# Optimization experiments

Measured on AMD Instinct MI355X. Metric: run time of the kernel, lower is better.

## Reference

```python
import jax, jax.numpy as jnp
import numpy as np

N, C_IN, C_OUT, W_DIM, H, W = 16, 512, 512, 512, 64, 64

def setup_inputs() -> dict:
    key = jax.random.key(0)
    ks = jax.random.split(key, 6)
    return {
        "x": jax.random.normal(ks[0], (N, C_IN, H, W), dtype=jnp.float32),
        "w": jax.random.normal(ks[1], (N, W_DIM), dtype=jnp.float32),
        "noise": jax.random.normal(ks[2], (N, 1, H, W), dtype=jnp.float32),
        "affine_w": jax.random.normal(ks[3], (C_IN, W_DIM), dtype=jnp.float32) * (1.0 / np.sqrt(W_DIM)),
        "affine_b": jnp.ones((C_IN,), dtype=jnp.float32),  # bias_init=1.0
        "noise_strength": jnp.ones((), dtype=jnp.float32),
        "conv_w": jax.random.normal(ks[4], (C_OUT, C_IN, 3, 3), dtype=jnp.float32),
        "conv_b": jnp.zeros((C_OUT,), dtype=jnp.float32),
    }

def reference(x, w, noise, affine_w, affine_b, noise_strength, conv_w, conv_b):
    # affine: s = w @ affine_w.T + affine_b  (no activation)
    s = jnp.einsum('nd,cd->nc', w, affine_w) + affine_b  # [N, C_in]
    # Demodulated per-sample conv. Original builds w_n = W * s_n then demodulates;
    # since conv is linear in the weight's input-channel scale, this is equivalent to
    # scaling the input by s and the output by the demod factor d.
    w2 = jnp.sum(conv_w * conv_w, axis=(2, 3))  # [O, I]: sum over kernel taps
    d = jax.lax.rsqrt(jnp.einsum('ni,oi->no', s * s, w2) + 1e-8)  # [N, O]
    x_mod = x * s[:, :, None, None]
    y = jax.lax.conv_general_dilated(
        x_mod, conv_w, window_strides=(1, 1), padding='SAME',
        dimension_numbers=('NCHW', 'OIHW', 'NCHW'))  # [N, O, H, W]
    y = y * d[:, :, None, None] + conv_b[None, :, None, None]
    y = y + noise * noise_strength
    return jnp.where(y >= 0, y, 0.2 * y)  # LeakyReLU(0.2)
```

## Files before the change

kernel.cpp:

```cpp
#include <hip/hip_runtime.h>
#include <hip/hip_bf16.h>

typedef unsigned short u16;
typedef short bf16x8 __attribute__((ext_vector_type(8)));
typedef float f32x4 __attribute__((ext_vector_type(4)));

#define N_    16
#define CIN   512
#define COUT  512
#define WD    512
#define P_    4096
#define CC    (COUT * CIN)

#define OFF_S   0u
#define OFF_D   32768u
#define OFF_Z   65536u
#define OFF_WBT 131072u
#define OFF_XB  8388608u
#define WS_NEED (OFF_XB + 67108864u)

__device__ __forceinline__ u16 f2bf(float f) {
  union { float f; unsigned u; } a; a.f = f;
  unsigned r = a.u + 0x7fffu + ((a.u >> 16) & 1u);
  return (u16)(r >> 16);
}

__device__ __forceinline__ void gl_lds16(const u16* g, u16* l) {
  __builtin_amdgcn_global_load_lds(
      (const __attribute__((address_space(1))) void*)g,
      (__attribute__((address_space(3))) void*)l, 16, 0, 0);
}

__global__ void k_zero(float* z) { z[threadIdx.x] = 0.f; }

__global__ __launch_bounds__(256) void k_affine(const float* __restrict__ w,
                                                const float* __restrict__ aw,
                                                const float* __restrict__ ab,
                                                float* __restrict__ s) {
  int idx = blockIdx.x * 256 + threadIdx.x;
  int n = idx >> 9, c = idx & 511;
  const float4* wr = (const float4*)(w + (size_t)n * WD);
  const float4* ar = (const float4*)(aw + (size_t)c * WD);
  float acc = 0.f;
#pragma unroll 4
  for (int k = 0; k < WD / 4; ++k) {
    float4 a = wr[k], b = ar[k];
    acc += a.x * b.x + a.y * b.y + a.z * b.z + a.w * b.w;
  }
  s[idx] = acc + ab[c];
}

__global__ __launch_bounds__(256) void k_demod(const float* __restrict__ s,
                                               const float* __restrict__ cw,
                                               float* __restrict__ d) {
  __shared__ float w2[CIN];
  int o = blockIdx.x;
  const float* wr = cw + (size_t)o * CIN * 9;
  for (int i = threadIdx.x; i < CIN; i += 256) {
    float acc = 0.f;
#pragma unroll
    for (int t = 0; t < 9; ++t) { float v = wr[i * 9 + t]; acc += v * v; }
    w2[i] = acc;
  }
  __syncthreads();
  int wave = threadIdx.x >> 6, lane = threadIdx.x & 63;
  for (int nn = wave; nn < N_; nn += 4) {
    float acc = 0.f;
    for (int i = lane; i < CIN; i += 64) {
      float sv = s[nn * CIN + i];
      acc += sv * sv * w2[i];
    }
#pragma unroll
    for (int off = 32; off > 0; off >>= 1) acc += __shfl_down(acc, off);
    if (lane == 0) {
      float a = acc + 1e-8f;
      float r = rsqrtf(a);
      r = r * (1.5f - 0.5f * a * r * r);
      d[nn * COUT + o] = r;
    }
  }
}

__global__ __launch_bounds__(256) void k_wprep(const float* __restrict__ cw,
                                               u16* __restrict__ wbt) {
  int idx = blockIdx.x * 256 + threadIdx.x;
  if (idx >= COUT * CIN * 9) return;
  int t = idx % 9; int oi = idx / 9; int i = oi & 511; int o = oi >> 9;
  wbt[((size_t)t * COUT + o) * CIN + i] = f2bf(cw[idx]);
}

__global__ __launch_bounds__(256) void k_xmod(const float* __restrict__ x,
                                              const float* __restrict__ s,
                                              u16* __restrict__ xb) {
  __shared__ float tile[64][65];
  int b = blockIdx.x;
  int pt = b & 63; int ct = (b >> 6) & 7; int n = b >> 9;
  int c0 = ct * 64, p0 = pt * 64;
  const float* xp = x + ((size_t)n * CIN + c0) * P_ + p0;
  int t = threadIdx.x;
#pragma unroll
  for (int pass = 0; pass < 4; ++pass) {
    int r = pass * 16 + (t >> 4);
    int col4 = (t & 15);
    float4 v = *(const float4*)(xp + (size_t)r * P_ + col4 * 4);
    float sc = s[n * CIN + c0 + r];
    tile[r][col4 * 4 + 0] = v.x * sc;
    tile[r][col4 * 4 + 1] = v.y * sc;
    tile[r][col4 * 4 + 2] = v.z * sc;
    tile[r][col4 * 4 + 3] = v.w * sc;
  }
  __syncthreads();
  int p = t >> 2, cq = (t & 3) * 16;
  union { u16 us[16]; uint4 q[2]; } pk;
#pragma unroll
  for (int j = 0; j < 16; ++j) pk.us[j] = f2bf(tile[cq + j][p]);
  uint4* dst = (uint4*)(xb + ((size_t)n * P_ + p0 + p) * CIN + c0 + cq);
  dst[0] = pk.q[0];
  dst[1] = pk.q[1];
}

__global__ __launch_bounds__(512, 1) void k_conv(const u16* __restrict__ xb,
                                                 const u16* __restrict__ wbt,
                                                 const u16* __restrict__ zp,
                                                 const float* __restrict__ dmod,
                                                 const float* __restrict__ cbias,
                                                 const float* __restrict__ noise,
                                                 const float* __restrict__ nstr,
                                                 float* __restrict__ out) {
  __shared__ u16 smA[4][8192];
  __shared__ u16 smB[4][8192];

  int bid = blockIdx.x;
  int wg = (bid & 7) * 64 + (bid >> 3);
  int n = wg >> 5;
  int rem = wg & 31;
  int ob = rem >> 4;
  int pb = rem & 15;

  int tid = threadIdx.x;
  int wv = tid >> 6, l = tid & 63;
  int wr = wv >> 2, wc = wv & 3;
  int lrow = l & 15, kgrp = l >> 4;
  int prs = kgrp ^ ((lrow >> 1) & 3);

  int srow = tid >> 2;
  int lslot = (tid & 3) ^ ((tid >> 3) & 3);
  const u16* xbn = xb + (size_t)n * P_ * CIN;
  int hg[2], wgp[2];
#pragma unroll
  for (int g = 0; g < 2; ++g) {
    int ploc = g * 128 + srow;
    hg[g] = pb * 4 + (ploc >> 6);
    wgp[g] = ploc & 63;
  }
  const u16* srcA_base[2];
#pragma unroll
  for (int g = 0; g < 2; ++g)
    srcA_base[g] = wbt + (size_t)(ob * 256 + g * 128 + srow) * CIN + lslot * 8;

  auto stage_A = [&](int tt) {
    int b = tt & 3;
    int tapn = tt >> 4, cbn = tt & 15;
#pragma unroll
    for (int g = 0; g < 2; ++g) {
      const u16* src = srcA_base[g] + (size_t)tapn * CC + cbn * 32;
      gl_lds16(src, &smA[b][g * 4096 + wv * 512]);
    }
  };
  auto bsrc_for_tap = [&](int tapn, int g) -> const u16* {
    int dh = tapn < 3 ? -1 : (tapn < 6 ? 0 : 1);
    int dw = tapn - (dh + 1) * 3 - 1;
    int hh = hg[g] + dh, ww = wgp[g] + dw;
    bool val = ((unsigned)hh < 64u) && ((unsigned)ww < 64u);
    return val ? (xbn + ((size_t)((hh << 6) + ww)) * CIN + lslot * 8)
               : (zp + lslot * 8);
  };
  auto stage_B = [&](int tt) {
    int b = tt & 3;
    int tapn = tt >> 4, cbn = tt & 15;
#pragma unroll
    for (int g = 0; g < 2; ++g)
      gl_lds16(bsrc_for_tap(tapn, g) + cbn * 32, &smB[b][g * 4096 + wv * 512]);
  };

  f32x4 acc0[4][4], acc1[4][4];
  f32x4 zero = {0.f, 0.f, 0.f, 0.f};
#pragma unroll
  for (int i = 0; i < 4; ++i)
#pragma unroll
    for (int j = 0; j < 4; ++j) { acc0[i][j] = zero; acc1[i][j] = zero; }

  stage_A(0); stage_B(0);
  stage_A(1); stage_B(1);
  stage_A(2); stage_B(2);

  int tap3 = 0, cb3 = 3;
  const u16* rpA[2];
  const u16* rpB[2];
#pragma unroll
  for (int g = 0; g < 2; ++g) {
    rpA[g] = srcA_base[g] + 3 * 32;
    rpB[g] = bsrc_for_tap(0, g) + 3 * 32;
  }

  for (int t = 0; t < 144; ++t) {
    int b = t & 3;
    int bs = (t + 3) & 3;
    if (t <= 141)      asm volatile("s_waitcnt vmcnt(8)" ::: "memory");
    else if (t == 142) asm volatile("s_waitcnt vmcnt(4)" ::: "memory");
    else               asm volatile("s_waitcnt vmcnt(0)" ::: "memory");
    __builtin_amdgcn_s_barrier();
    __builtin_amdgcn_sched_barrier(0);

    const u16* A = smA[b];
    const u16* B = smB[b];

    bf16x8 Bf[4], Af0[4], Af1[4];
#pragma unroll
    for (int ni = 0; ni < 4; ++ni)
      Bf[ni] = *(const bf16x8*)&B[(wc * 64 + ni * 16 + lrow) * 32 + prs * 8];
#pragma unroll
    for (int mi = 0; mi < 4; ++mi)
      Af0[mi] = *(const bf16x8*)&A[(wr * 128 + mi * 16 + lrow) * 32 + prs * 8];
    __builtin_amdgcn_sched_barrier(0);
#pragma unroll
    for (int mi = 0; mi < 4; ++mi)
      Af1[mi] = *(const bf16x8*)&A[(wr * 128 + 64 + mi * 16 + lrow) * 32 + prs * 8];

    if (t <= 140) {
#pragma unroll
      for (int g = 0; g < 2; ++g)
        gl_lds16(rpA[g], &smA[bs][g * 4096 + wv * 512]);
#pragma unroll
      for (int g = 0; g < 2; ++g)
        gl_lds16(rpB[g], &smB[bs][g * 4096 + wv * 512]);
      cb3++;
      if (cb3 == 16) {
        cb3 = 0; tap3++;
#pragma unroll
        for (int g = 0; g < 2; ++g) {
          rpA[g] = srcA_base[g] + (size_t)tap3 * CC;
          rpB[g] = bsrc_for_tap(tap3, g);
        }
      } else {
#pragma unroll
        for (int g = 0; g < 2; ++g) { rpA[g] += 32; rpB[g] += 32; }
      }
    }

    asm volatile("s_waitcnt lgkmcnt(4)" ::: "memory");
    __builtin_amdgcn_sched_barrier(0);
    __builtin_amdgcn_s_setprio(1);
#pragma unroll
    for (int mi = 0; mi < 4; ++mi)
#pragma unroll
      for (int ni = 0; ni < 4; ++ni)
        acc0[mi][ni] = __builtin_amdgcn_mfma_f32_16x16x32_bf16(
            Af0[mi], Bf[ni], acc0[mi][ni], 0, 0, 0);
    __builtin_amdgcn_s_setprio(0);

    asm volatile("s_waitcnt lgkmcnt(0)" ::: "memory");
    __builtin_amdgcn_sched_barrier(0);
    __builtin_amdgcn_s_setprio(1);
#pragma unroll
    for (int mi = 0; mi < 4; ++mi)
#pragma unroll
      for (int ni = 0; ni < 4; ++ni)
        acc1[mi][ni] = __builtin_amdgcn_mfma_f32_16x16x32_bf16(
            Af1[mi], Bf[ni], acc1[mi][ni], 0, 0, 0);
    __builtin_amdgcn_s_setprio(0);
  }

  float ns = nstr[0];
  const float* noise_n = noise + (size_t)n * P_;
  float nz[4];
#pragma unroll
  for (int ni = 0; ni < 4; ++ni)
    nz[ni] = noise_n[pb * 256 + wc * 64 + ni * 16 + lrow] * ns;

  auto epi = [&](f32x4 (&A_)[4][4], int qm) {
#pragma unroll
    for (int mi = 0; mi < 4; ++mi) {
      int o0 = ob * 256 + wr * 128 + qm * 64 + mi * 16 + kgrp * 4;
#pragma unroll
      for (int r = 0; r < 4; ++r) {
        int o = o0 + r;
        float dv = dmod[n * COUT + o];
        float bv = cbias[o];
        float* orow = out + ((size_t)(n * COUT + o)) * P_ + pb * 256 + wc * 64;
#pragma unroll
        for (int ni = 0; ni < 4; ++ni) {
          float v = A_[mi][ni][r] * dv + bv + nz[ni];
          orow[ni * 16 + lrow] = v >= 0.f ? v : 0.2f * v;
        }
      }
    }
  };
  epi(acc0, 0);
  epi(acc1, 1);
}

__global__ __launch_bounds__(64) void k_conv_naive(const float* __restrict__ x,
                                                   const float* __restrict__ cw,
                                                   const float* __restrict__ cbias,
                                                   const float* __restrict__ noise,
                                                   const float* __restrict__ nstr,
                                                   const float* __restrict__ s,
                                                   const float* __restrict__ d,
                                                   float* __restrict__ out) {
  int bid = blockIdx.x;
  int h = bid & 63; int o = (bid >> 6) & 511; int n = bid >> 15;
  int wcol = threadIdx.x;
  float acc = 0.f;
  for (int i = 0; i < CIN; ++i) {
    float sv = s[n * CIN + i];
    const float* xrow = x + ((size_t)(n * CIN + i)) * P_;
    const float* wrp = cw + ((size_t)o * CIN + i) * 9;
#pragma unroll
    for (int t = 0; t < 9; ++t) {
      int hh = h + t / 3 - 1, ww = wcol + t % 3 - 1;
      float xv = ((unsigned)hh < 64u && (unsigned)ww < 64u) ? xrow[hh * 64 + ww] : 0.f;
      acc += xv * sv * wrp[t];
    }
  }
  float v = acc * d[n * COUT + o] + cbias[o] + noise[(size_t)n * P_ + h * 64 + wcol] * nstr[0];
  out[((size_t)(n * COUT + o)) * P_ + h * 64 + wcol] = v >= 0.f ? v : 0.2f * v;
}

extern "C" void kernel_launch(void* const* d_in, const int* in_sizes, int n_in,
                              void* d_out, int out_size, void* d_ws, size_t ws_size,
                              hipStream_t stream) {
  const float* x    = (const float*)d_in[0];
  const float* w    = (const float*)d_in[1];
  const float* noise= (const float*)d_in[2];
  const float* aw   = (const float*)d_in[3];
  const float* ab   = (const float*)d_in[4];
  const float* nstr = (const float*)d_in[5];
  const float* cw   = (const float*)d_in[6];
  const float* cb   = (const float*)d_in[7];
  float* out = (float*)d_out;
  char* ws = (char*)d_ws;
  float* s = (float*)(ws + OFF_S);
  float* d = (float*)(ws + OFF_D);

  k_affine<<<(N_ * COUT) / 256, 256, 0, stream>>>(w, aw, ab, s);
  k_demod<<<COUT, 256, 0, stream>>>(s, cw, d);

  if (ws_size >= WS_NEED) {
    u16* zp  = (u16*)(ws + OFF_Z);
    u16* wbt = (u16*)(ws + OFF_WBT);
    u16* xbb = (u16*)(ws + OFF_XB);
    k_zero<<<1, 256, 0, stream>>>((float*)zp);
    k_wprep<<<(COUT * CIN * 9 + 255) / 256, 256, 0, stream>>>(cw, wbt);
    k_xmod<<<N_ * 8 * 64, 256, 0, stream>>>(x, s, xbb);
    k_conv<<<512, 512, 0, stream>>>(xbb, wbt, zp, d, cb, noise, nstr, out);
  } else {
    k_conv_naive<<<N_ * COUT * 64, 64, 0, stream>>>(x, cw, cb, noise, nstr, s, d, out);
  }
}
```

Baseline: 340.7 us.

## Load conv weight fragments straight into registers and drop the LDS A buffer

The weight (A) operand is no longer staged through shared memory. Each wave loads its own weight fragments from global memory directly into a double-buffered register set, one k-step ahead, while only the activation (B) tiles keep the 4-stage LDS ring. The loop is unrolled by two so the register buffers can swap roles, the MFMA loop is reordered to wait on B reads one at a time, and launch bounds now ask for two blocks per CU. This removes the A-side LDS traffic and halves shared memory use, but raises register pressure (128 accumulators plus 64 registers of prefetched A), which risks spills under the 2-block bound. Weight reads also become less coalesced per-lane global loads that rely on cache.

```diff
diff --git a/kernel.cpp b/kernel.cpp
--- a/kernel.cpp
+++ b/kernel.cpp
@@ -119,7 +119,7 @@
   dst[1] = pk.q[1];
 }
 
-__global__ __launch_bounds__(512, 1) void k_conv(const u16* __restrict__ xb,
+__global__ __launch_bounds__(512, 2) void k_conv(const u16* __restrict__ xb,
                                                  const u16* __restrict__ wbt,
                                                  const u16* __restrict__ zp,
                                                  const float* __restrict__ dmod,
@@ -127,7 +127,6 @@
                                                  const float* __restrict__ noise,
                                                  const float* __restrict__ nstr,
                                                  float* __restrict__ out) {
-  __shared__ u16 smA[4][8192];
   __shared__ u16 smB[4][8192];
 
   int bid = blockIdx.x;
@@ -153,20 +152,7 @@
     hg[g] = pb * 4 + (ploc >> 6);
     wgp[g] = ploc & 63;
   }
-  const u16* srcA_base[2];
-#pragma unroll
-  for (int g = 0; g < 2; ++g)
-    srcA_base[g] = wbt + (size_t)(ob * 256 + g * 128 + srow) * CIN + lslot * 8;
-
-  auto stage_A = [&](int tt) {
-    int b = tt & 3;
-    int tapn = tt >> 4, cbn = tt & 15;
-#pragma unroll
-    for (int g = 0; g < 2; ++g) {
-      const u16* src = srcA_base[g] + (size_t)tapn * CC + cbn * 32;
-      gl_lds16(src, &smA[b][g * 4096 + wv * 512]);
-    }
-  };
+
   auto bsrc_for_tap = [&](int tapn, int g) -> const u16* {
     int dh = tapn < 3 ? -1 : (tapn < 6 ? 0 : 1);
     int dw = tapn - (dh + 1) * 3 - 1;
@@ -183,6 +169,15 @@
       gl_lds16(bsrc_for_tap(tapn, g) + cbn * 32, &smB[b][g * 4096 + wv * 512]);
   };
 
+  const u16* wbtA = wbt + (size_t)(ob * 256 + wr * 128 + lrow) * CIN + kgrp * 8;
+  auto loadAf = [&](bf16x8 (&L)[8], int tau) {
+    int tapN = tau >> 4, cbN = tau & 15;
+    const u16* p = wbtA + (size_t)tapN * CC + cbN * 32;
+#pragma unroll
+    for (int mi = 0; mi < 8; ++mi)
+      L[mi] = *(const bf16x8*)(p + mi * 16 * CIN);
+  };
+
   f32x4 acc0[4][4], acc1[4][4];
   f32x4 zero = {0.f, 0.f, 0.f, 0.f};
 #pragma unroll
@@ -190,47 +185,37 @@
 #pragma unroll
     for (int j = 0; j < 4; ++j) { acc0[i][j] = zero; acc1[i][j] = zero; }
 
-  stage_A(0); stage_B(0);
-  stage_A(1); stage_B(1);
-  stage_A(2); stage_B(2);
+  bf16x8 AfA[8], AfB[8];
+
+  stage_B(0);
+  loadAf(AfA, 0);
+  stage_B(1);
+  stage_B(2);
 
   int tap3 = 0, cb3 = 3;
-  const u16* rpA[2];
   const u16* rpB[2];
 #pragma unroll
-  for (int g = 0; g < 2; ++g) {
-    rpA[g] = srcA_base[g] + 3 * 32;
-    rpB[g] = bsrc_for_tap(0, g) + 3 * 32;
-  }
-
-  for (int t = 0; t < 144; ++t) {
-    int b = t & 3;
-    int bs = (t + 3) & 3;
-    if (t <= 141)      asm volatile("s_waitcnt vmcnt(8)" ::: "memory");
-    else if (t == 142) asm volatile("s_waitcnt vmcnt(4)" ::: "memory");
-    else               asm volatile("s_waitcnt vmcnt(0)" ::: "memory");
+  for (int g = 0; g < 2; ++g) rpB[g] = bsrc_for_tap(0, g) + 3 * 32;
+
+  auto body = [&](int tau, bf16x8 (&U)[8], bf16x8 (&L)[8]) {
+    int b = tau & 3;
+    int bs = (tau + 3) & 3;
+    if (tau == 0)        asm volatile("s_waitcnt vmcnt(4)" ::: "memory");
+    else if (tau <= 141) asm volatile("s_waitcnt vmcnt(2)" ::: "memory");
+    else                 asm volatile("s_waitcnt vmcnt(0)" ::: "memory");
     __builtin_amdgcn_s_barrier();
     __builtin_amdgcn_sched_barrier(0);
 
-    const u16* A = smA[b];
     const u16* B = smB[b];
-
-    bf16x8 Bf[4], Af0[4], Af1[4];
+    bf16x8 Bf[4];
 #pragma unroll
     for (int ni = 0; ni < 4; ++ni)
       Bf[ni] = *(const bf16x8*)&B[(wc * 64 + ni * 16 + lrow) * 32 + prs * 8];
-#pragma unroll
-    for (int mi = 0; mi < 4; ++mi)
-      Af0[mi] = *(const bf16x8*)&A[(wr * 128 + mi * 16 + lrow) * 32 + prs * 8];
     __builtin_amdgcn_sched_barrier(0);
-#pragma unroll
-    for (int mi = 0; mi < 4; ++mi)
-      Af1[mi] = *(const bf16x8*)&A[(wr * 128 + 64 + mi * 16 + lrow) * 32 + prs * 8];
-
-    if (t <= 140) {
-#pragma unroll
-      for (int g = 0; g < 2; ++g)
-        gl_lds16(rpA[g], &smA[bs][g * 4096 + wv * 512]);
+
+    if (tau <= 142) loadAf(L, tau + 1);
+    __builtin_amdgcn_sched_barrier(0);
+    if (tau <= 140) {
 #pragma unroll
       for (int g = 0; g < 2; ++g)
         gl_lds16(rpB[g], &smB[bs][g * 4096 + wv * 512]);
@@ -238,37 +223,37 @@
       if (cb3 == 16) {
         cb3 = 0; tap3++;
 #pragma unroll
-        for (int g = 0; g < 2; ++g) {
-          rpA[g] = srcA_base[g] + (size_t)tap3 * CC;
-          rpB[g] = bsrc_for_tap(tap3, g);
-        }
+        for (int g = 0; g < 2; ++g) rpB[g] = bsrc_for_tap(tap3, g);
       } else {
 #pragma unroll
-        for (int g = 0; g < 2; ++g) { rpA[g] += 32; rpB[g] += 32; }
+        for (int g = 0; g < 2; ++g) rpB[g] += 32;
       }
     }
-
-    asm volatile("s_waitcnt lgkmcnt(4)" ::: "memory");
     __builtin_amdgcn_sched_barrier(0);
+
     __builtin_amdgcn_s_setprio(1);
 #pragma unroll
-    for (int mi = 0; mi < 4; ++mi)
-#pragma unroll
-      for (int ni = 0; ni < 4; ++ni)
+    for (int ni = 0; ni < 4; ++ni) {
+      if (ni == 0)      asm volatile("s_waitcnt lgkmcnt(3)" ::: "memory");
+      else if (ni == 1) asm volatile("s_waitcnt lgkmcnt(2)" ::: "memory");
+      else if (ni == 2) asm volatile("s_waitcnt lgkmcnt(1)" ::: "memory");
+      else              asm volatile("s_waitcnt lgkmcnt(0)" ::: "memory");
+      __builtin_amdgcn_sched_barrier(0);
+#pragma unroll
+      for (int mi = 0; mi < 4; ++mi)
         acc0[mi][ni] = __builtin_amdgcn_mfma_f32_16x16x32_bf16(
-            Af0[mi], Bf[ni], acc0[mi][ni], 0, 0, 0);
+            U[mi], Bf[ni], acc0[mi][ni], 0, 0, 0);
+#pragma unroll
+      for (int mi = 0; mi < 4; ++mi)
+        acc1[mi][ni] = __builtin_amdgcn_mfma_f32_16x16x32_bf16(
+            U[mi + 4], Bf[ni], acc1[mi][ni], 0, 0, 0);
+    }
     __builtin_amdgcn_s_setprio(0);
-
-    asm volatile("s_waitcnt lgkmcnt(0)" ::: "memory");
-    __builtin_amdgcn_sched_barrier(0);
-    __builtin_amdgcn_s_setprio(1);
-#pragma unroll
-    for (int mi = 0; mi < 4; ++mi)
-#pragma unroll
-      for (int ni = 0; ni < 4; ++ni)
-        acc1[mi][ni] = __builtin_amdgcn_mfma_f32_16x16x32_bf16(
-            Af1[mi], Bf[ni], acc1[mi][ni], 0, 0, 0);
-    __builtin_amdgcn_s_setprio(0);
+  };
+
+  for (int t = 0; t < 144; t += 2) {
+    body(t, AfA, AfB);
+    body(t + 1, AfB, AfA);
   }
 
   float ns = nstr[0];
```

Result: slower. 739.7 us (+117.1%).

## Shrink conv tile to 256x128 with 4 waves and triple-buffer LDS for two blocks per CU

Applied to the files above, without the earlier changes.

The implicit-GEMM conv block changes from 512 threads computing a 256x256 output tile with 4-stage LDS buffering to 256 threads computing a 256x128 tile (two image rows) with 3-stage buffering. LDS per block drops so two blocks can be resident per CU, and the grid doubles to 1024 blocks. The aim is better latency hiding through inter-block overlap and better load balance across CUs. The cost is a lower arithmetic intensity per tile, since the weight tile A is now reloaded for twice as many blocks, and a shallower prefetch depth.

```diff
diff --git a/kernel.cpp b/kernel.cpp
--- a/kernel.cpp
+++ b/kernel.cpp
@@ -119,7 +119,7 @@
   dst[1] = pk.q[1];
 }
 
-__global__ __launch_bounds__(512, 1) void k_conv(const u16* __restrict__ xb,
+__global__ __launch_bounds__(256, 2) void k_conv(const u16* __restrict__ xb,
                                                  const u16* __restrict__ wbt,
                                                  const u16* __restrict__ zp,
                                                  const float* __restrict__ dmod,
@@ -127,60 +127,49 @@
                                                  const float* __restrict__ noise,
                                                  const float* __restrict__ nstr,
                                                  float* __restrict__ out) {
-  __shared__ u16 smA[4][8192];
-  __shared__ u16 smB[4][8192];
+  __shared__ u16 smA[3][8192];
+  __shared__ u16 smB[3][4096];
 
   int bid = blockIdx.x;
-  int wg = (bid & 7) * 64 + (bid >> 3);
-  int n = wg >> 5;
-  int rem = wg & 31;
-  int ob = rem >> 4;
-  int pb = rem & 15;
+  int wg = (bid & 7) * 128 + (bid >> 3);
+  int n = wg >> 6;
+  int rem = wg & 63;
+  int ob = rem >> 5;
+  int pb = rem & 31;
 
   int tid = threadIdx.x;
   int wv = tid >> 6, l = tid & 63;
-  int wr = wv >> 2, wc = wv & 3;
+  int wr = wv >> 1, wc = wv & 1;
   int lrow = l & 15, kgrp = l >> 4;
   int prs = kgrp ^ ((lrow >> 1) & 3);
 
-  int srow = tid >> 2;
-  int lslot = (tid & 3) ^ ((tid >> 3) & 3);
+  int rowbase = (wv << 4) + (l >> 2);
+  int kslot = (l & 3) ^ ((l >> 3) & 3);
   const u16* xbn = xb + (size_t)n * P_ * CIN;
-  int hg[2], wgp[2];
-#pragma unroll
-  for (int g = 0; g < 2; ++g) {
-    int ploc = g * 128 + srow;
-    hg[g] = pb * 4 + (ploc >> 6);
-    wgp[g] = ploc & 63;
-  }
-  const u16* srcA_base[2];
-#pragma unroll
-  for (int g = 0; g < 2; ++g)
-    srcA_base[g] = wbt + (size_t)(ob * 256 + g * 128 + srow) * CIN + lslot * 8;
-
-  auto stage_A = [&](int tt) {
-    int b = tt & 3;
-    int tapn = tt >> 4, cbn = tt & 15;
-#pragma unroll
-    for (int g = 0; g < 2; ++g) {
-      const u16* src = srcA_base[g] + (size_t)tapn * CC + cbn * 32;
-      gl_lds16(src, &smA[b][g * 4096 + wv * 512]);
-    }
-  };
-  auto bsrc_for_tap = [&](int tapn, int g) -> const u16* {
+
+  const u16* baseA = wbt + (size_t)(ob * 256 + rowbase) * CIN + kslot * 8;
+
+  auto bsrc_for_tap = [&](int tapn, int c) -> const u16* {
     int dh = tapn < 3 ? -1 : (tapn < 6 ? 0 : 1);
     int dw = tapn - (dh + 1) * 3 - 1;
-    int hh = hg[g] + dh, ww = wgp[g] + dw;
+    int hh = pb * 2 + c + dh, ww = rowbase + dw;
     bool val = ((unsigned)hh < 64u) && ((unsigned)ww < 64u);
-    return val ? (xbn + ((size_t)((hh << 6) + ww)) * CIN + lslot * 8)
-               : (zp + lslot * 8);
+    return val ? (xbn + ((size_t)((hh << 6) + ww)) * CIN + kslot * 8)
+               : (zp + kslot * 8);
   };
-  auto stage_B = [&](int tt) {
-    int b = tt & 3;
+
+  auto stage_A = [&](int tt, int buf) {
     int tapn = tt >> 4, cbn = tt & 15;
-#pragma unroll
-    for (int g = 0; g < 2; ++g)
-      gl_lds16(bsrc_for_tap(tapn, g) + cbn * 32, &smB[b][g * 4096 + wv * 512]);
+    const u16* p = baseA + (size_t)tapn * CC + cbn * 32;
+#pragma unroll
+    for (int c = 0; c < 4; ++c)
+      gl_lds16(p + c * 64 * CIN, &smA[buf][c * 2048 + wv * 512]);
+  };
+  auto stage_B = [&](int tt, int buf) {
+    int tapn = tt >> 4, cbn = tt & 15;
+#pragma unroll
+    for (int c = 0; c < 2; ++c)
+      gl_lds16(bsrc_for_tap(tapn, c) + cbn * 32, &smB[buf][c * 2048 + wv * 512]);
   };
 
   f32x4 acc0[4][4], acc1[4][4];
@@ -190,30 +179,24 @@
 #pragma unroll
     for (int j = 0; j < 4; ++j) { acc0[i][j] = zero; acc1[i][j] = zero; }
 
-  stage_A(0); stage_B(0);
-  stage_A(1); stage_B(1);
-  stage_A(2); stage_B(2);
-
-  int tap3 = 0, cb3 = 3;
-  const u16* rpA[2];
+  stage_A(0, 0); stage_B(0, 0);
+  stage_A(1, 1); stage_B(1, 1);
+
+  int tap3 = 0, cb3 = 2;
+  const u16* rpA = baseA + 2 * 32;
   const u16* rpB[2];
 #pragma unroll
-  for (int g = 0; g < 2; ++g) {
-    rpA[g] = srcA_base[g] + 3 * 32;
-    rpB[g] = bsrc_for_tap(0, g) + 3 * 32;
-  }
-
+  for (int c = 0; c < 2; ++c) rpB[c] = bsrc_for_tap(0, c) + 2 * 32;
+
+  int bcur = 0, bstg = 2;
   for (int t = 0; t < 144; ++t) {
-    int b = t & 3;
-    int bs = (t + 3) & 3;
-    if (t <= 141)      asm volatile("s_waitcnt vmcnt(8)" ::: "memory");
-    else if (t == 142) asm volatile("s_waitcnt vmcnt(4)" ::: "memory");
-    else               asm volatile("s_waitcnt vmcnt(0)" ::: "memory");
+    if (t <= 142) asm volatile("s_waitcnt vmcnt(6)" ::: "memory");
+    else          asm volatile("s_waitcnt vmcnt(0)" ::: "memory");
     __builtin_amdgcn_s_barrier();
     __builtin_amdgcn_sched_barrier(0);
 
-    const u16* A = smA[b];
-    const u16* B = smB[b];
+    const u16* A = smA[bcur];
+    const u16* B = smB[bcur];
 
     bf16x8 Bf[4], Af0[4], Af1[4];
 #pragma unroll
@@ -227,24 +210,23 @@
     for (int mi = 0; mi < 4; ++mi)
       Af1[mi] = *(const bf16x8*)&A[(wr * 128 + 64 + mi * 16 + lrow) * 32 + prs * 8];
 
-    if (t <= 140) {
-#pragma unroll
-      for (int g = 0; g < 2; ++g)
-        gl_lds16(rpA[g], &smA[bs][g * 4096 + wv * 512]);
-#pragma unroll
-      for (int g = 0; g < 2; ++g)
-        gl_lds16(rpB[g], &smB[bs][g * 4096 + wv * 512]);
+    if (t <= 141) {
+#pragma unroll
+      for (int c = 0; c < 4; ++c)
+        gl_lds16(rpA + c * 64 * CIN, &smA[bstg][c * 2048 + wv * 512]);
+#pragma unroll
+      for (int c = 0; c < 2; ++c)
+        gl_lds16(rpB[c], &smB[bstg][c * 2048 + wv * 512]);
       cb3++;
       if (cb3 == 16) {
         cb3 = 0; tap3++;
-#pragma unroll
-        for (int g = 0; g < 2; ++g) {
-          rpA[g] = srcA_base[g] + (size_t)tap3 * CC;
-          rpB[g] = bsrc_for_tap(tap3, g);
-        }
+        rpA = baseA + (size_t)tap3 * CC;
+#pragma unroll
+        for (int c = 0; c < 2; ++c) rpB[c] = bsrc_for_tap(tap3, c);
       } else {
-#pragma unroll
-        for (int g = 0; g < 2; ++g) { rpA[g] += 32; rpB[g] += 32; }
+        rpA += 32;
+#pragma unroll
+        for (int c = 0; c < 2; ++c) rpB[c] += 32;
       }
     }
 
@@ -269,6 +251,9 @@
         acc1[mi][ni] = __builtin_amdgcn_mfma_f32_16x16x32_bf16(
             Af1[mi], Bf[ni], acc1[mi][ni], 0, 0, 0);
     __builtin_amdgcn_s_setprio(0);
+
+    bcur = (bcur == 2) ? 0 : bcur + 1;
+    bstg = (bstg == 2) ? 0 : bstg + 1;
   }
 
   float ns = nstr[0];
@@ -276,7 +261,7 @@
   float nz[4];
 #pragma unroll
   for (int ni = 0; ni < 4; ++ni)
-    nz[ni] = noise_n[pb * 256 + wc * 64 + ni * 16 + lrow] * ns;
+    nz[ni] = noise_n[pb * 128 + wc * 64 + ni * 16 + lrow] * ns;
 
   auto epi = [&](f32x4 (&A_)[4][4], int qm) {
 #pragma unroll
@@ -287,7 +272,7 @@
         int o = o0 + r;
         float dv = dmod[n * COUT + o];
         float bv = cbias[o];
-        float* orow = out + ((size_t)(n * COUT + o)) * P_ + pb * 256 + wc * 64;
+        float* orow = out + ((size_t)(n * COUT + o)) * P_ + pb * 128 + wc * 64;
 #pragma unroll
         for (int ni = 0; ni < 4; ++ni) {
           float v = A_[mi][ni][r] * dv + bv + nz[ni];
@@ -353,7 +338,7 @@
     k_zero<<<1, 256, 0, stream>>>((float*)zp);
     k_wprep<<<(COUT * CIN * 9 + 255) / 256, 256, 0, stream>>>(cw, wbt);
     k_xmod<<<N_ * 8 * 64, 256, 0, stream>>>(x, s, xbb);
-    k_conv<<<512, 512, 0, stream>>>(xbb, wbt, zp, d, cb, noise, nstr, out);
+    k_conv<<<1024, 256, 0, stream>>>(xbb, wbt, zp, d, cb, noise, nstr, out);
   } else {
     k_conv_naive<<<N_ * COUT * 64, 64, 0, stream>>>(x, cw, cb, noise, nstr, s, d, out);
   }
```

New measurement: 358.7 us. 5.3% more time.

## Double-buffer LDS fragments in registers across K iterations and request two blocks per CU

Applied to the files above, without the earlier changes.

Unrolls the main conv GEMM loop by two and keeps two register sets of A and B fragments. The next stage's LDS reads are issued before the current stage's MFMAs, so LDS latency overlaps with matrix math. The vmcnt and lgkmcnt waits and the barrier placement are reworked to match. Launch bounds now ask for two blocks per CU. That roughly halves the register budget while the extra fragment sets add pressure, so spills are a real risk. The kernel's LDS use probably still blocks a second resident block.

```diff
diff --git a/kernel.cpp b/kernel.cpp
--- a/kernel.cpp
+++ b/kernel.cpp
@@ -119,7 +119,7 @@
   dst[1] = pk.q[1];
 }
 
-__global__ __launch_bounds__(512, 1) void k_conv(const u16* __restrict__ xb,
+__global__ __launch_bounds__(512, 2) void k_conv(const u16* __restrict__ xb,
                                                  const u16* __restrict__ wbt,
                                                  const u16* __restrict__ zp,
                                                  const float* __restrict__ dmod,
@@ -190,6 +190,8 @@
 #pragma unroll
     for (int j = 0; j < 4; ++j) { acc0[i][j] = zero; acc1[i][j] = zero; }
 
+  bf16x8 BfA[4], A0A[4], A1A[4], BfB[4], A0B[4], A1B[4];
+
   stage_A(0); stage_B(0);
   stage_A(1); stage_B(1);
   stage_A(2); stage_B(2);
@@ -203,29 +205,45 @@
     rpB[g] = bsrc_for_tap(0, g) + 3 * 32;
   }
 
-  for (int t = 0; t < 144; ++t) {
-    int b = t & 3;
+  asm volatile("s_waitcnt vmcnt(8)" ::: "memory");
+  __builtin_amdgcn_s_barrier();
+  __builtin_amdgcn_sched_barrier(0);
+  {
+    const u16* A = smA[0];
+    const u16* B = smB[0];
+#pragma unroll
+    for (int ni = 0; ni < 4; ++ni)
+      BfA[ni] = *(const bf16x8*)&B[(wc * 64 + ni * 16 + lrow) * 32 + prs * 8];
+#pragma unroll
+    for (int mi = 0; mi < 4; ++mi)
+      A0A[mi] = *(const bf16x8*)&A[(wr * 128 + mi * 16 + lrow) * 32 + prs * 8];
+#pragma unroll
+    for (int mi = 0; mi < 4; ++mi)
+      A1A[mi] = *(const bf16x8*)&A[(wr * 128 + 64 + mi * 16 + lrow) * 32 + prs * 8];
+  }
+  __builtin_amdgcn_sched_barrier(0);
+
+  auto body = [&](int t,
+                  bf16x8 (&Bfc)[4], bf16x8 (&A0c)[4], bf16x8 (&A1c)[4],
+                  bf16x8 (&Bfn)[4], bf16x8 (&A0n)[4], bf16x8 (&A1n)[4]) {
+    int bn = (t + 1) & 3;
     int bs = (t + 3) & 3;
-    if (t <= 141)      asm volatile("s_waitcnt vmcnt(8)" ::: "memory");
-    else if (t == 142) asm volatile("s_waitcnt vmcnt(4)" ::: "memory");
-    else               asm volatile("s_waitcnt vmcnt(0)" ::: "memory");
-    __builtin_amdgcn_s_barrier();
-    __builtin_amdgcn_sched_barrier(0);
-
-    const u16* A = smA[b];
-    const u16* B = smB[b];
-
-    bf16x8 Bf[4], Af0[4], Af1[4];
-#pragma unroll
-    for (int ni = 0; ni < 4; ++ni)
-      Bf[ni] = *(const bf16x8*)&B[(wc * 64 + ni * 16 + lrow) * 32 + prs * 8];
-#pragma unroll
-    for (int mi = 0; mi < 4; ++mi)
-      Af0[mi] = *(const bf16x8*)&A[(wr * 128 + mi * 16 + lrow) * 32 + prs * 8];
-    __builtin_amdgcn_sched_barrier(0);
-#pragma unroll
-    for (int mi = 0; mi < 4; ++mi)
-      Af1[mi] = *(const bf16x8*)&A[(wr * 128 + 64 + mi * 16 + lrow) * 32 + prs * 8];
+
+    if (t < 143) {
+      if (t == 142) asm volatile("s_waitcnt vmcnt(0)" ::: "memory");
+      else          asm volatile("s_waitcnt vmcnt(4)" ::: "memory");
+      __builtin_amdgcn_s_barrier();
+      __builtin_amdgcn_sched_barrier(0);
+      const u16* An = smA[bn];
+      const u16* Bn = smB[bn];
+#pragma unroll
+      for (int ni = 0; ni < 4; ++ni)
+        Bfn[ni] = *(const bf16x8*)&Bn[(wc * 64 + ni * 16 + lrow) * 32 + prs * 8];
+#pragma unroll
+      for (int mi = 0; mi < 4; ++mi)
+        A0n[mi] = *(const bf16x8*)&An[(wr * 128 + mi * 16 + lrow) * 32 + prs * 8];
+      __builtin_amdgcn_sched_barrier(0);
+    }
 
     if (t <= 140) {
 #pragma unroll
@@ -246,29 +264,43 @@
 #pragma unroll
         for (int g = 0; g < 2; ++g) { rpA[g] += 32; rpB[g] += 32; }
       }
-    }
-
-    asm volatile("s_waitcnt lgkmcnt(4)" ::: "memory");
+      __builtin_amdgcn_sched_barrier(0);
+    }
+
+    if (t < 143) asm volatile("s_waitcnt lgkmcnt(8)" ::: "memory");
+    else         asm volatile("s_waitcnt lgkmcnt(0)" ::: "memory");
     __builtin_amdgcn_sched_barrier(0);
+
     __builtin_amdgcn_s_setprio(1);
 #pragma unroll
     for (int mi = 0; mi < 4; ++mi)
 #pragma unroll
       for (int ni = 0; ni < 4; ++ni)
         acc0[mi][ni] = __builtin_amdgcn_mfma_f32_16x16x32_bf16(
-            Af0[mi], Bf[ni], acc0[mi][ni], 0, 0, 0);
+            A0c[mi], Bfc[ni], acc0[mi][ni], 0, 0, 0);
     __builtin_amdgcn_s_setprio(0);
 
-    asm volatile("s_waitcnt lgkmcnt(0)" ::: "memory");
-    __builtin_amdgcn_sched_barrier(0);
+    if (t < 143) {
+      const u16* An = smA[bn];
+#pragma unroll
+      for (int mi = 0; mi < 4; ++mi)
+        A1n[mi] = *(const bf16x8*)&An[(wr * 128 + 64 + mi * 16 + lrow) * 32 + prs * 8];
+      __builtin_amdgcn_sched_barrier(0);
+    }
+
     __builtin_amdgcn_s_setprio(1);
 #pragma unroll
     for (int mi = 0; mi < 4; ++mi)
 #pragma unroll
       for (int ni = 0; ni < 4; ++ni)
         acc1[mi][ni] = __builtin_amdgcn_mfma_f32_16x16x32_bf16(
-            Af1[mi], Bf[ni], acc1[mi][ni], 0, 0, 0);
+            A1c[mi], Bfc[ni], acc1[mi][ni], 0, 0, 0);
     __builtin_amdgcn_s_setprio(0);
+  };
+
+  for (int t = 0; t < 144; t += 2) {
+    body(t,     BfA, A0A, A1A, BfB, A0B, A1B);
+    body(t + 1, BfB, A0B, A1B, BfA, A0A, A1A);
   }
 
   float ns = nstr[0];
```

Result: slower. 355.6 us (+4.4%).
